# Kernel tuning notes

Hardware: AMD Instinct MI355X
Metric: run time of the kernel (lower is better)

The kernel has to match this reference:

```python
import jax, jax.numpy as jnp
import numpy as np
import math

N_NODES = 50000
N_EDGES = 500000
D = 128
H = 8
HD = D // H
N_RELS = 200


def setup_inputs() -> dict:
    key = jax.random.key(0)
    ks = jax.random.split(key, 12)
    return {
        "q": jax.random.normal(ks[0], (N_NODES, D), jnp.float32),
        "E": jax.random.normal(ks[1], (N_NODES, D), jnp.float32),
        "R_emb": jax.random.normal(ks[2], (N_RELS, D), jnp.float32),
        "Wq": jax.random.normal(ks[3], (D, D), jnp.float32) / math.sqrt(D),
        "Wk": jax.random.normal(ks[4], (D, D), jnp.float32) / math.sqrt(D),
        "Wv": jax.random.normal(ks[5], (D, D), jnp.float32) / math.sqrt(D),
        "Wo": jax.random.normal(ks[6], (4 * D, D), jnp.float32) / math.sqrt(4 * D),
        "ln_g": jnp.ones((D,), jnp.float32),
        "ln_b": jnp.zeros((D,), jnp.float32),
        "deg_scale": jax.random.uniform(ks[7], (N_EDGES,), jnp.float32) + 0.5,
        "edge_src": jax.random.randint(ks[8], (N_EDGES,), 0, N_NODES),
        "edge_rel": jax.random.randint(ks[9], (N_EDGES,), 0, N_RELS),
        "edge_dst": jax.random.randint(ks[10], (N_EDGES,), 0, N_NODES),
    }


def reference(q, E, R_emb, Wq, Wk, Wv, Wo, ln_g, ln_b, deg_scale,
              edge_src, edge_rel, edge_dst):
    n = q.shape[0]
    # DistMult message: ent * rel per edge   [E, D]
    msg = E[edge_src] * R_emb[edge_rel]
    # scatter multi-head sigmoid attention (query_expand = edge_dst)
    k = (msg @ Wk).reshape(-1, H, HD)                      # [E, H, hd]
    qe = (q @ Wq)[edge_dst].reshape(-1, H, HD)             # [E, H, hd]
    alphas = (qe * k).sum(-1) / math.sqrt(HD)              # [E, H]
    w = jax.nn.sigmoid(alphas)                             # sigmoid attention
    v = (msg @ Wv).reshape(-1, H, HD)                      # [E, H, hd]
    scaled_v = (w[..., None] * v).reshape(-1, D)           # [E, D]
    # simple_pna: scalars={'scaled'} (v * deg_scale), aggs=[mean,max,min,std]
    x = scaled_v * deg_scale[:, None]                      # [E, D]
    seg = edge_dst
    s = jax.ops.segment_sum(x, seg, num_segments=n)        # sum
    cnt = jax.ops.segment_sum(jnp.ones((x.shape[0],), x.dtype), seg, num_segments=n)
    nonempty = (cnt > 0)[:, None]
    mean = jnp.where(nonempty, s / jnp.maximum(cnt, 1.0)[:, None], 0.0)
    mx = jax.ops.segment_max(x, seg, num_segments=n)
    mx = jnp.where(nonempty, mx, 0.0)                      # empty segs -> 0 (torch zeros init)
    mn = jax.ops.segment_min(x, seg, num_segments=n)
    mn = jnp.where(nonempty, mn, 0.0)
    sq = jax.ops.segment_sum(x * x, seg, num_segments=n)
    std = jnp.sqrt(jnp.maximum(sq - s * s, 1e-8))          # matches (sq_agg - sum_agg**2).clamp_min(1e-8).sqrt()
    agg = jnp.concatenate([mean, mx, mn, std], axis=-1)    # [N, 4D]
    out = agg @ Wo                                         # [N, D]
    # GatedResidueNorm, use_gate=False: residual add + LayerNorm
    h = out + q
    mu = h.mean(-1, keepdims=True)
    var = ((h - mu) ** 2).mean(-1, keepdims=True)
    return (h - mu) * jax.lax.rsqrt(var + 1e-5) * ln_g + ln_b
```

## Files before the change

kernel.cpp:

```cpp
#include <hip/hip_runtime.h>

#define D 128

typedef __attribute__((ext_vector_type(8))) short short8;
typedef __attribute__((ext_vector_type(4))) float floatx4;

union __align__(16) U8 { unsigned short u[8]; short8 v; };

__device__ __forceinline__ unsigned enc_f(float f) {
    unsigned u = __float_as_uint(f);
    return (u & 0x80000000u) ? ~u : (u | 0x80000000u);
}
__device__ __forceinline__ float dec_f(unsigned u) {
    return (u & 0x80000000u) ? __uint_as_float(u ^ 0x80000000u) : __uint_as_float(~u);
}
__device__ __forceinline__ unsigned short f2bf(float f) {
    unsigned u = __float_as_uint(f);
    unsigned r = (u + 0x7FFFu + ((u >> 16) & 1u)) >> 16;
    return (unsigned short)r;
}
__device__ __forceinline__ float bf2f(unsigned short s) {
    return __uint_as_float(((unsigned)s) << 16);
}


__global__ void init_kernel(float* __restrict__ sum, float* __restrict__ sumsq,
                            unsigned* __restrict__ mxe, unsigned* __restrict__ mne,
                            int* __restrict__ cnt, int* __restrict__ fill, int nNodes) {
    int i = blockIdx.x * blockDim.x + threadIdx.x;
    int total = nNodes * D;
    if (i < total) {
        sum[i] = 0.f;
        sumsq[i] = 0.f;
        mxe[i] = 0u;
        mne[i] = 0xFFFFFFFFu;
    }
    if (i < nNodes) { cnt[i] = 0; fill[i] = 0; }
}


__global__ void hist_kernel(const int* __restrict__ dst, int* __restrict__ cnt, int nE) {
    int i = blockIdx.x * blockDim.x + threadIdx.x;
    if (i < nE) atomicAdd(&cnt[dst[i]], 1);
}

__global__ void scanA_kernel(const int* __restrict__ cnt, int* __restrict__ chunksum, int n) {
    __shared__ int sm[256];
    int t = threadIdx.x;
    int i = blockIdx.x * 256 + t;
    sm[t] = (i < n) ? cnt[i] : 0;
    __syncthreads();
    for (int s = 128; s > 0; s >>= 1) {
        if (t < s) sm[t] += sm[t + s];
        __syncthreads();
    }
    if (t == 0) chunksum[blockIdx.x] = sm[0];
}

__global__ void scanB_kernel(const int* __restrict__ chunksum, int* __restrict__ chunkoff, int nc) {
    __shared__ int sm[256];
    int t = threadIdx.x;
    int v = (t < nc) ? chunksum[t] : 0;
    sm[t] = v;
    __syncthreads();
    for (int s = 1; s < 256; s <<= 1) {
        int add = (t >= s) ? sm[t - s] : 0;
        __syncthreads();
        sm[t] += add;
        __syncthreads();
    }
    if (t < nc) chunkoff[t] = sm[t] - v;
}

__global__ void scanC_kernel(const int* __restrict__ cnt, const int* __restrict__ chunkoff,
                             int* __restrict__ off, int n) {
    __shared__ int sm[256];
    int t = threadIdx.x;
    int i = blockIdx.x * 256 + t;
    int v = (i < n) ? cnt[i] : 0;
    sm[t] = v;
    __syncthreads();
    for (int s = 1; s < 256; s <<= 1) {
        int add = (t >= s) ? sm[t - s] : 0;
        __syncthreads();
        sm[t] += add;
        __syncthreads();
    }
    if (i < n) off[i] = chunkoff[blockIdx.x] + sm[t] - v;
}

__global__ void scatter_kernel(const int* __restrict__ dst, const int* __restrict__ off,
                               int* __restrict__ fill, int* __restrict__ perm, int nE) {
    int i = blockIdx.x * blockDim.x + threadIdx.x;
    if (i < nE) {
        int d = dst[i];
        int p = off[d] + atomicAdd(&fill[d], 1);
        perm[p] = i;
    }
}


__global__ void pack_kernel(const float* __restrict__ W0, const float* __restrict__ W1,
                            int Kdim, unsigned short* __restrict__ hi,
                            unsigned short* __restrict__ lo) {
    int ksn = Kdim >> 5;
    int nt = blockIdx.x / ksn;
    int ks = blockIdx.x % ksn;
    int l = threadIdx.x;
    int c = nt * 16 + (l & 15);
    const float* Wsrc = (c < 128) ? W0 : W1;
    int cc = c & 127;
    int kbase = ks * 32 + (l >> 4) * 8;
    size_t o = ((size_t)blockIdx.x * 64 + l) * 8;
#pragma unroll
    for (int j = 0; j < 8; ++j) {
        float w = Wsrc[(size_t)(kbase + j) * 128 + cc];
        unsigned short h = f2bf(w);
        hi[o + j] = h;
        if (lo) lo[o + j] = f2bf(w - bf2f(h));
    }
}


__global__ __launch_bounds__(256, 2) void qproj_mfma(
        const float* __restrict__ q,
        const unsigned short* __restrict__ Bhi, const unsigned short* __restrict__ Blo,
        unsigned short* __restrict__ qp, int nNodes) {
    __shared__ __align__(16) unsigned short qhi[64][128];
    __shared__ __align__(16) unsigned short qlo[64][128];
    int t = threadIdx.x;
    int n0 = blockIdx.x * 64;
    {
        int e = t >> 2, sub = t & 3;
        int node = n0 + e;
        for (int cc = 0; cc < 4; ++cc) {
            int chunk = sub * 4 + cc;
            U8 H, L;
            if (node < nNodes) {
                const float* srcp = q + (size_t)node * 128 + chunk * 8;
                float4 v0 = *(const float4*)(srcp);
                float4 v1 = *(const float4*)(srcp + 4);
                float vv[8] = {v0.x, v0.y, v0.z, v0.w, v1.x, v1.y, v1.z, v1.w};
#pragma unroll
                for (int j = 0; j < 8; ++j) {
                    unsigned short h = f2bf(vv[j]);
                    H.u[j] = h; L.u[j] = f2bf(vv[j] - bf2f(h));
                }
            } else {
#pragma unroll
                for (int j = 0; j < 8; ++j) { H.u[j] = 0; L.u[j] = 0; }
            }
            int sc = chunk ^ (e & 7);
            *reinterpret_cast<short8*>(&qhi[e][sc * 8]) = H.v;
            *reinterpret_cast<short8*>(&qlo[e][sc * 8]) = L.v;
        }
    }
    __syncthreads();
    int w = t >> 6, l = t & 63;
    int lrow = l & 15, lk = l >> 4;
    floatx4 acc[4][2];
#pragma unroll
    for (int mt = 0; mt < 4; ++mt)
#pragma unroll
        for (int n = 0; n < 2; ++n) acc[mt][n] = (floatx4){0.f, 0.f, 0.f, 0.f};
    for (int ks = 0; ks < 4; ++ks) {
        short8 ah[4], al[4];
#pragma unroll
        for (int mt = 0; mt < 4; ++mt) {
            int row = mt * 16 + lrow;
            int sc = (ks * 4 + lk) ^ (row & 7);
            ah[mt] = *reinterpret_cast<const short8*>(&qhi[row][sc * 8]);
            al[mt] = *reinterpret_cast<const short8*>(&qlo[row][sc * 8]);
        }
#pragma unroll
        for (int ntl = 0; ntl < 2; ++ntl) {
            int ntg = w * 2 + ntl;
            size_t bo = ((size_t)(ntg * 4 + ks) * 64 + l) * 8;
            short8 bh = *reinterpret_cast<const short8*>(Bhi + bo);
            short8 bl = *reinterpret_cast<const short8*>(Blo + bo);
#pragma unroll
            for (int mt = 0; mt < 4; ++mt) {
                acc[mt][ntl] = __builtin_amdgcn_mfma_f32_16x16x32_bf16(ah[mt], bh, acc[mt][ntl], 0, 0, 0);
                acc[mt][ntl] = __builtin_amdgcn_mfma_f32_16x16x32_bf16(al[mt], bh, acc[mt][ntl], 0, 0, 0);
                acc[mt][ntl] = __builtin_amdgcn_mfma_f32_16x16x32_bf16(ah[mt], bl, acc[mt][ntl], 0, 0, 0);
            }
        }
    }
#pragma unroll
    for (int mt = 0; mt < 4; ++mt)
#pragma unroll
        for (int ntl = 0; ntl < 2; ++ntl) {
            int col = (w * 2 + ntl) * 16 + lrow;
#pragma unroll
            for (int r = 0; r < 4; ++r) {
                int row = mt * 16 + lk * 4 + r;
                int node = n0 + row;
                if (node < nNodes) qp[(size_t)node * 128 + col] = f2bf(acc[mt][ntl][r]);
            }
        }
}


__device__ __forceinline__ void flush1(float* __restrict__ sum, float* __restrict__ sumsq,
                                       unsigned* __restrict__ mxe, unsigned* __restrict__ mne,
                                       int node, int col, float s, float q2, float mx, float mn) {
    size_t b = (size_t)node * 128 + col;
    atomicAdd(&sum[b], s);
    atomicAdd(&sumsq[b], q2);
    atomicMax(&mxe[b], enc_f(mx));
    atomicMin(&mne[b], enc_f(mn));
}

__global__ __launch_bounds__(256, 2) void edge_mfma(
        const float* __restrict__ E, const float* __restrict__ R,
        const unsigned short* __restrict__ qp,
        const unsigned short* __restrict__ Bhi, const unsigned short* __restrict__ Blo,
        const float* __restrict__ deg,
        const int* __restrict__ src, const int* __restrict__ rel,
        const int* __restrict__ dst, const int* __restrict__ perm,
        float* __restrict__ sum, float* __restrict__ sumsq,
        unsigned* __restrict__ mxe, unsigned* __restrict__ mne, int nE) {

    __shared__ __align__(16) unsigned short msgb[2][64][128];
    __shared__ __align__(16) unsigned short Kb[64][128];
    __shared__ float alph[64][8];
    __shared__ int sdst[64];
    __shared__ float sdegs[64];

    int t = threadIdx.x;
    int e0 = blockIdx.x * 64;

    if (t < 64) {
        int ei = e0 + t;
        if (ei < nE) { int p = perm[ei]; sdst[t] = dst[p]; sdegs[t] = deg[p]; }
        else { sdst[t] = -1; sdegs[t] = 0.f; }
    }
    {
        int e = t >> 2, sub = t & 3;
        int ei = e0 + e;
        bool ok = ei < nE;
        int p = ok ? perm[ei] : 0;
        const float* Erow = E + (size_t)(ok ? src[p] : 0) * 128;
        const float* Rrow = R + (size_t)(ok ? rel[p] : 0) * 128;
        for (int cc = 0; cc < 4; ++cc) {
            int chunk = sub * 4 + cc;
            U8 H, L;
            if (ok) {
                float4 a0 = *(const float4*)(Erow + chunk * 8);
                float4 a1 = *(const float4*)(Erow + chunk * 8 + 4);
                float4 b0 = *(const float4*)(Rrow + chunk * 8);
                float4 b1 = *(const float4*)(Rrow + chunk * 8 + 4);
                float m[8] = {a0.x * b0.x, a0.y * b0.y, a0.z * b0.z, a0.w * b0.w,
                              a1.x * b1.x, a1.y * b1.y, a1.z * b1.z, a1.w * b1.w};
#pragma unroll
                for (int j = 0; j < 8; ++j) {
                    unsigned short h = f2bf(m[j]);
                    H.u[j] = h; L.u[j] = f2bf(m[j] - bf2f(h));
                }
            } else {
#pragma unroll
                for (int j = 0; j < 8; ++j) { H.u[j] = 0; L.u[j] = 0; }
            }
            int sc = chunk ^ (e & 7);
            *reinterpret_cast<short8*>(&msgb[0][e][sc * 8]) = H.v;
            *reinterpret_cast<short8*>(&msgb[1][e][sc * 8]) = L.v;
        }
    }
    __syncthreads();

    int w = t >> 6, l = t & 63;
    int lrow = l & 15, lk = l >> 4;
    int colbase = w * 64;
    floatx4 acc[4][4];
#pragma unroll
    for (int mt = 0; mt < 4; ++mt)
#pragma unroll
        for (int n = 0; n < 4; ++n) acc[mt][n] = (floatx4){0.f, 0.f, 0.f, 0.f};

    for (int ks = 0; ks < 4; ++ks) {
        short8 ah[4], al[4];
#pragma unroll
        for (int mt = 0; mt < 4; ++mt) {
            int row = mt * 16 + lrow;
            int sc = (ks * 4 + lk) ^ (row & 7);
            ah[mt] = *reinterpret_cast<const short8*>(&msgb[0][row][sc * 8]);
            al[mt] = *reinterpret_cast<const short8*>(&msgb[1][row][sc * 8]);
        }
#pragma unroll
        for (int ntl = 0; ntl < 4; ++ntl) {
            int ntg = w * 4 + ntl;
            size_t bo = ((size_t)(ntg * 4 + ks) * 64 + l) * 8;
            short8 bh = *reinterpret_cast<const short8*>(Bhi + bo);
            short8 bl = *reinterpret_cast<const short8*>(Blo + bo);
#pragma unroll
            for (int mt = 0; mt < 4; ++mt) {
                acc[mt][ntl] = __builtin_amdgcn_mfma_f32_16x16x32_bf16(ah[mt], bh, acc[mt][ntl], 0, 0, 0);
                acc[mt][ntl] = __builtin_amdgcn_mfma_f32_16x16x32_bf16(al[mt], bh, acc[mt][ntl], 0, 0, 0);
                acc[mt][ntl] = __builtin_amdgcn_mfma_f32_16x16x32_bf16(ah[mt], bl, acc[mt][ntl], 0, 0, 0);
            }
        }
    }
    __syncthreads();

    float* Vlds = (float*)msgb;
#pragma unroll
    for (int mt = 0; mt < 4; ++mt)
#pragma unroll
        for (int ntl = 0; ntl < 4; ++ntl) {
            int col = colbase + ntl * 16 + lrow;
#pragma unroll
            for (int r = 0; r < 4; ++r) {
                int row = mt * 16 + lk * 4 + r;
                int key = ((row >> 2) & 3) << 4;
                float vvv = acc[mt][ntl][r];
                if (col < 128) Kb[row][col ^ key] = f2bf(vvv);
                else Vlds[row * 128 + ((col - 128) ^ key)] = vvv;
            }
        }
    __syncthreads();

    {
        int e = t >> 2, h2 = (t & 3) * 2;
        int dn = sdst[e];
        int key = ((e >> 2) & 3) << 4;
#pragma unroll
        for (int hh = 0; hh < 2; ++hh) {
            int h = h2 + hh;
            float wgt = 0.f;
            if (dn >= 0) {
                int cb = (h * 16) ^ key;
                U8 k0, k1, q0, q1;
                k0.v = *reinterpret_cast<const short8*>(&Kb[e][cb]);
                k1.v = *reinterpret_cast<const short8*>(&Kb[e][cb + 8]);
                const unsigned short* qrow = qp + (size_t)dn * 128 + h * 16;
                q0.v = *reinterpret_cast<const short8*>(qrow);
                q1.v = *reinterpret_cast<const short8*>(qrow + 8);
                float a = 0.f;
#pragma unroll
                for (int j = 0; j < 8; ++j) {
                    a = fmaf(bf2f(k0.u[j]), bf2f(q0.u[j]), a);
                    a = fmaf(bf2f(k1.u[j]), bf2f(q1.u[j]), a);
                }
                float alpha = a * 0.25f;
                wgt = 1.f / (1.f + __expf(-alpha));
            }
            alph[e][h] = wgt;
        }
    }
    __syncthreads();

    {
        int col = t & 127, seg = t >> 7;
        int eb = seg * 32, ee = eb + 32;
        float s = 0.f, q2 = 0.f, mx = 0.f, mn = 0.f;
        int run = -1;
        for (int e = eb; e < ee; ++e) {
            int dnv = sdst[e];
            if (dnv < 0) {
                if (run >= 0) { flush1(sum, sumsq, mxe, mne, run, col, s, q2, mx, mn); run = -1; }
                continue;
            }
            int key = ((e >> 2) & 3) << 4;
            float x = Vlds[e * 128 + (col ^ key)] * alph[e][col >> 4] * sdegs[e];
            if (dnv != run) {
                if (run >= 0) flush1(sum, sumsq, mxe, mne, run, col, s, q2, mx, mn);
                run = dnv;
                s = x; q2 = x * x; mx = x; mn = x;
            } else {
                s += x; q2 = fmaf(x, x, q2);
                mx = fmaxf(mx, x); mn = fminf(mn, x);
            }
        }
        if (run >= 0) flush1(sum, sumsq, mxe, mne, run, col, s, q2, mx, mn);
    }
}


__global__ __launch_bounds__(256, 2) void finalize_mfma(
        const float* __restrict__ sum, const float* __restrict__ sumsq,
        const unsigned* __restrict__ mxe, const unsigned* __restrict__ mne,
        const int* __restrict__ cnt, const unsigned short* __restrict__ Wop,
        const float* __restrict__ q, const float* __restrict__ ln_g,
        const float* __restrict__ ln_b, float* __restrict__ out, int nNodes) {
    __shared__ __align__(16) unsigned short aggb[32][512];
    int t = threadIdx.x;
    int n0 = blockIdx.x * 32;
    {
        int nl = t >> 3, part = t & 7;
        int node = n0 + nl;
        int c0 = part * 16;
        U8 Mh[2], Xh[2], Nh[2], Sh[2];
        if (node < nNodes) {
            int c = cnt[node];
            float invc = (c > 0) ? 1.f / (float)c : 0.f;
            size_t b0 = (size_t)node * 128 + c0;
#pragma unroll
            for (int g = 0; g < 2; ++g) {
                float4 s0 = *(const float4*)(sum + b0 + g * 8);
                float4 s1 = *(const float4*)(sum + b0 + g * 8 + 4);
                float4 t0 = *(const float4*)(sumsq + b0 + g * 8);
                float4 t1 = *(const float4*)(sumsq + b0 + g * 8 + 4);
                uint4 x0 = *(const uint4*)(mxe + b0 + g * 8);
                uint4 x1 = *(const uint4*)(mxe + b0 + g * 8 + 4);
                uint4 m0 = *(const uint4*)(mne + b0 + g * 8);
                uint4 m1 = *(const uint4*)(mne + b0 + g * 8 + 4);
                float ss[8] = {s0.x, s0.y, s0.z, s0.w, s1.x, s1.y, s1.z, s1.w};
                float qq[8] = {t0.x, t0.y, t0.z, t0.w, t1.x, t1.y, t1.z, t1.w};
                unsigned xx[8] = {x0.x, x0.y, x0.z, x0.w, x1.x, x1.y, x1.z, x1.w};
                unsigned nn[8] = {m0.x, m0.y, m0.z, m0.w, m1.x, m1.y, m1.z, m1.w};
#pragma unroll
                for (int j = 0; j < 8; ++j) {
                    float s = ss[j];
                    float mean = s * invc;
                    float mxv = (c > 0) ? dec_f(xx[j]) : 0.f;
                    float mnv = (c > 0) ? dec_f(nn[j]) : 0.f;
                    float sd = sqrtf(fmaxf(qq[j] - s * s, 1e-8f));
                    Mh[g].u[j] = f2bf(mean);
                    Xh[g].u[j] = f2bf(mxv);
                    Nh[g].u[j] = f2bf(mnv);
                    Sh[g].u[j] = f2bf(sd);
                }
            }
        } else {
#pragma unroll
            for (int g = 0; g < 2; ++g)
#pragma unroll
                for (int j = 0; j < 8; ++j) { Mh[g].u[j] = 0; Xh[g].u[j] = 0; Nh[g].u[j] = 0; Sh[g].u[j] = 0; }
        }
#pragma unroll
        for (int g = 0; g < 2; ++g) {
            int base = part * 2 + g, k = nl & 7, ch;
            ch = (0 * 16 + base) ^ k; *reinterpret_cast<short8*>(&aggb[nl][ch * 8]) = Mh[g].v;
            ch = (1 * 16 + base) ^ k; *reinterpret_cast<short8*>(&aggb[nl][ch * 8]) = Xh[g].v;
            ch = (2 * 16 + base) ^ k; *reinterpret_cast<short8*>(&aggb[nl][ch * 8]) = Nh[g].v;
            ch = (3 * 16 + base) ^ k; *reinterpret_cast<short8*>(&aggb[nl][ch * 8]) = Sh[g].v;
        }
    }
    __syncthreads();

    int w = t >> 6, l = t & 63;
    int lrow = l & 15, lk = l >> 4;
    floatx4 acc[2][2];
#pragma unroll
    for (int mt = 0; mt < 2; ++mt)
#pragma unroll
        for (int n = 0; n < 2; ++n) acc[mt][n] = (floatx4){0.f, 0.f, 0.f, 0.f};
    for (int ks = 0; ks < 16; ++ks) {
        short8 a[2];
#pragma unroll
        for (int mt = 0; mt < 2; ++mt) {
            int row = mt * 16 + lrow;
            int ch = (ks * 4 + lk) ^ (row & 7);
            a[mt] = *reinterpret_cast<const short8*>(&aggb[row][ch * 8]);
        }
#pragma unroll
        for (int ntl = 0; ntl < 2; ++ntl) {
            int ntg = w * 2 + ntl;
            short8 b = *reinterpret_cast<const short8*>(Wop + ((size_t)(ntg * 16 + ks) * 64 + l) * 8);
#pragma unroll
            for (int mt = 0; mt < 2; ++mt)
                acc[mt][ntl] = __builtin_amdgcn_mfma_f32_16x16x32_bf16(a[mt], b, acc[mt][ntl], 0, 0, 0);
        }
    }
    __syncthreads();

    float* hb = (float*)aggb;
#pragma unroll
    for (int mt = 0; mt < 2; ++mt)
#pragma unroll
        for (int ntl = 0; ntl < 2; ++ntl) {
            int col = (w * 2 + ntl) * 16 + lrow;
#pragma unroll
            for (int r = 0; r < 4; ++r) {
                int row = mt * 16 + lk * 4 + r;
                int node = n0 + row;
                float h = acc[mt][ntl][r] + ((node < nNodes) ? q[(size_t)node * 128 + col] : 0.f);
                int key = ((row >> 2) & 3) << 4;
                hb[row * 128 + (col ^ key)] = h;
            }
        }
    __syncthreads();

    {
        int nl = t >> 3, part = t & 7;
        int node = n0 + nl;
        int key = ((nl >> 2) & 3) << 4;
        int c0 = part * 16;
        int cb = c0 ^ key;
        const float* hrow = hb + nl * 128;
        float4 h0 = *(const float4*)(hrow + cb);
        float4 h1 = *(const float4*)(hrow + cb + 4);
        float4 h2 = *(const float4*)(hrow + cb + 8);
        float4 h3 = *(const float4*)(hrow + cb + 12);
        float ps = h0.x + h0.y + h0.z + h0.w + h1.x + h1.y + h1.z + h1.w
                 + h2.x + h2.y + h2.z + h2.w + h3.x + h3.y + h3.z + h3.w;
        ps += __shfl_xor(ps, 1);
        ps += __shfl_xor(ps, 2);
        ps += __shfl_xor(ps, 4);
        float mu = ps * (1.f / 128.f);
        float d0x = h0.x - mu, d0y = h0.y - mu, d0z = h0.z - mu, d0w = h0.w - mu;
        float d1x = h1.x - mu, d1y = h1.y - mu, d1z = h1.z - mu, d1w = h1.w - mu;
        float d2x = h2.x - mu, d2y = h2.y - mu, d2z = h2.z - mu, d2w = h2.w - mu;
        float d3x = h3.x - mu, d3y = h3.y - mu, d3z = h3.z - mu, d3w = h3.w - mu;
        float pv = d0x*d0x + d0y*d0y + d0z*d0z + d0w*d0w
                 + d1x*d1x + d1y*d1y + d1z*d1z + d1w*d1w
                 + d2x*d2x + d2y*d2y + d2z*d2z + d2w*d2w
                 + d3x*d3x + d3y*d3y + d3z*d3z + d3w*d3w;
        pv += __shfl_xor(pv, 1);
        pv += __shfl_xor(pv, 2);
        pv += __shfl_xor(pv, 4);
        float rr = rsqrtf(pv * (1.f / 128.f) + 1e-5f);
        if (node < nNodes) {
            float4 g0 = *(const float4*)(ln_g + c0);
            float4 g1 = *(const float4*)(ln_g + c0 + 4);
            float4 g2 = *(const float4*)(ln_g + c0 + 8);
            float4 g3 = *(const float4*)(ln_g + c0 + 12);
            float4 b0 = *(const float4*)(ln_b + c0);
            float4 b1 = *(const float4*)(ln_b + c0 + 4);
            float4 b2 = *(const float4*)(ln_b + c0 + 8);
            float4 b3 = *(const float4*)(ln_b + c0 + 12);
            float* orow = out + (size_t)node * 128 + c0;
            float4 o;
            o.x = d0x * rr * g0.x + b0.x; o.y = d0y * rr * g0.y + b0.y;
            o.z = d0z * rr * g0.z + b0.z; o.w = d0w * rr * g0.w + b0.w;
            *(float4*)(orow) = o;
            o.x = d1x * rr * g1.x + b1.x; o.y = d1y * rr * g1.y + b1.y;
            o.z = d1z * rr * g1.z + b1.z; o.w = d1w * rr * g1.w + b1.w;
            *(float4*)(orow + 4) = o;
            o.x = d2x * rr * g2.x + b2.x; o.y = d2y * rr * g2.y + b2.y;
            o.z = d2z * rr * g2.z + b2.z; o.w = d2w * rr * g2.w + b2.w;
            *(float4*)(orow + 8) = o;
            o.x = d3x * rr * g3.x + b3.x; o.y = d3y * rr * g3.y + b3.y;
            o.z = d3z * rr * g3.z + b3.z; o.w = d3w * rr * g3.w + b3.w;
            *(float4*)(orow + 12) = o;
        }
    }
}


extern "C" void kernel_launch(void* const* d_in, const int* in_sizes, int n_in,
                              void* d_out, int out_size, void* d_ws, size_t ws_size,
                              hipStream_t stream) {
    const float* q    = (const float*)d_in[0];
    const float* E    = (const float*)d_in[1];
    const float* R    = (const float*)d_in[2];
    const float* Wq   = (const float*)d_in[3];
    const float* Wk   = (const float*)d_in[4];
    const float* Wv   = (const float*)d_in[5];
    const float* Wo   = (const float*)d_in[6];
    const float* ln_g = (const float*)d_in[7];
    const float* ln_b = (const float*)d_in[8];
    const float* deg  = (const float*)d_in[9];
    const int* src    = (const int*)d_in[10];
    const int* rel    = (const int*)d_in[11];
    const int* dst    = (const int*)d_in[12];
    int nNodes = in_sizes[0] / D;
    int nEdges = in_sizes[10];
    float* out = (float*)d_out;

    char* w = (char*)d_ws;
    size_t nd = (size_t)nNodes * D;
    float* sum    = (float*)w;               w += nd * 4;
    float* sumsq  = (float*)w;               w += nd * 4;
    unsigned* mxe = (unsigned*)w;            w += nd * 4;
    unsigned* mne = (unsigned*)w;            w += nd * 4;
    unsigned short* qp = (unsigned short*)w; w += nd * 2;
    int* cnt      = (int*)w;                 w += (size_t)nNodes * 4;
    int* off      = (int*)w;                 w += (size_t)nNodes * 4;
    int* fill     = (int*)w;                 w += (size_t)nNodes * 4;
    int* perm     = (int*)w;                 w += (size_t)nEdges * 4;
    int* chunksum = (int*)w;                 w += 256 * 4;
    int* chunkoff = (int*)w;                 w += 256 * 4;
    unsigned short* Wp_hi  = (unsigned short*)w; w += 16 * 4 * 64 * 8 * 2;
    unsigned short* Wp_lo  = (unsigned short*)w; w += 16 * 4 * 64 * 8 * 2;
    unsigned short* Wqp_hi = (unsigned short*)w; w += 8 * 4 * 64 * 8 * 2;
    unsigned short* Wqp_lo = (unsigned short*)w; w += 8 * 4 * 64 * 8 * 2;
    unsigned short* Wop    = (unsigned short*)w; w += 8 * 16 * 64 * 8 * 2;

    int nChunks = (nNodes + 255) / 256;

    init_kernel<<<(int)((nd + 255) / 256), 256, 0, stream>>>(sum, sumsq, mxe, mne, cnt, fill, nNodes);
    hist_kernel<<<(nEdges + 255) / 256, 256, 0, stream>>>(dst, cnt, nEdges);
    scanA_kernel<<<nChunks, 256, 0, stream>>>(cnt, chunksum, nNodes);
    scanB_kernel<<<1, 256, 0, stream>>>(chunksum, chunkoff, nChunks);
    scanC_kernel<<<nChunks, 256, 0, stream>>>(cnt, chunkoff, off, nNodes);
    scatter_kernel<<<(nEdges + 255) / 256, 256, 0, stream>>>(dst, off, fill, perm, nEdges);

    pack_kernel<<<16 * 4, 64, 0, stream>>>(Wk, Wv, 128, Wp_hi, Wp_lo);
    pack_kernel<<<8 * 4, 64, 0, stream>>>(Wq, Wq, 128, Wqp_hi, Wqp_lo);
    pack_kernel<<<8 * 16, 64, 0, stream>>>(Wo, Wo, 512, Wop, (unsigned short*)nullptr);

    qproj_mfma<<<(nNodes + 63) / 64, 256, 0, stream>>>(q, Wqp_hi, Wqp_lo, qp, nNodes);
    edge_mfma<<<(nEdges + 63) / 64, 256, 0, stream>>>(E, R, qp, Wp_hi, Wp_lo, deg,
                                                      src, rel, dst, perm,
                                                      sum, sumsq, mxe, mne, nEdges);
    finalize_mfma<<<(nNodes + 31) / 32, 256, 0, stream>>>(sum, sumsq, mxe, mne, cnt, Wop,
                                                          q, ln_g, ln_b, out, nNodes);
}
```

Baseline: 546.1 us.

## Fuse edge processing, aggregation and output projection into a per-node-block kernel

Replaces the edge-parallel kernel, which scattered partial aggregates into global buffers with atomics, and the separate finalize kernel with one kernel that owns 8 destination nodes per block. Each block walks its sorted edge range in chunks of 32, does the K/V MFMA and the sigmoid attention, and reduces sum, sumsq, max and min in registers. It then applies the Wo projection and LayerNorm directly. This removes the big init pass, the global atomics and the round trip of the intermediate aggregates, at the cost of uneven per-block work, small partly padded MFMA tiles, and an MFMA M-tile of 16 when only 8 rows are valid.

```diff
diff --git a/kernel.cpp b/kernel.cpp
--- a/kernel.cpp
+++ b/kernel.cpp
@@ -1,19 +1,13 @@
 #include <hip/hip_runtime.h>
 
 #define D 128
+#define FLT_BIG 3.402823466e+38f
 
 typedef __attribute__((ext_vector_type(8))) short short8;
 typedef __attribute__((ext_vector_type(4))) float floatx4;
 
 union __align__(16) U8 { unsigned short u[8]; short8 v; };
 
-__device__ __forceinline__ unsigned enc_f(float f) {
-    unsigned u = __float_as_uint(f);
-    return (u & 0x80000000u) ? ~u : (u | 0x80000000u);
-}
-__device__ __forceinline__ float dec_f(unsigned u) {
-    return (u & 0x80000000u) ? __uint_as_float(u ^ 0x80000000u) : __uint_as_float(~u);
-}
 __device__ __forceinline__ unsigned short f2bf(float f) {
     unsigned u = __float_as_uint(f);
     unsigned r = (u + 0x7FFFu + ((u >> 16) & 1u)) >> 16;
@@ -24,20 +18,10 @@
 }
 
 
-__global__ void init_kernel(float* __restrict__ sum, float* __restrict__ sumsq,
-                            unsigned* __restrict__ mxe, unsigned* __restrict__ mne,
-                            int* __restrict__ cnt, int* __restrict__ fill, int nNodes) {
+__global__ void zero2_kernel(int* __restrict__ cnt, int* __restrict__ fill, int n) {
     int i = blockIdx.x * blockDim.x + threadIdx.x;
-    int total = nNodes * D;
-    if (i < total) {
-        sum[i] = 0.f;
-        sumsq[i] = 0.f;
-        mxe[i] = 0u;
-        mne[i] = 0xFFFFFFFFu;
-    }
-    if (i < nNodes) { cnt[i] = 0; fill[i] = 0; }
-}
-
+    if (i < n) { cnt[i] = 0; fill[i] = 0; }
+}
 
 __global__ void hist_kernel(const int* __restrict__ dst, int* __restrict__ cnt, int nE) {
     int i = blockIdx.x * blockDim.x + threadIdx.x;
@@ -201,338 +185,271 @@
 }
 
 
-__device__ __forceinline__ void flush1(float* __restrict__ sum, float* __restrict__ sumsq,
-                                       unsigned* __restrict__ mxe, unsigned* __restrict__ mne,
-                                       int node, int col, float s, float q2, float mx, float mn) {
-    size_t b = (size_t)node * 128 + col;
-    atomicAdd(&sum[b], s);
-    atomicAdd(&sumsq[b], q2);
-    atomicMax(&mxe[b], enc_f(mx));
-    atomicMin(&mne[b], enc_f(mn));
-}
-
-__global__ __launch_bounds__(256, 2) void edge_mfma(
+__global__ __launch_bounds__(256, 4) void edge_fused(
         const float* __restrict__ E, const float* __restrict__ R,
         const unsigned short* __restrict__ qp,
         const unsigned short* __restrict__ Bhi, const unsigned short* __restrict__ Blo,
+        const unsigned short* __restrict__ Wop,
         const float* __restrict__ deg,
         const int* __restrict__ src, const int* __restrict__ rel,
         const int* __restrict__ dst, const int* __restrict__ perm,
-        float* __restrict__ sum, float* __restrict__ sumsq,
-        unsigned* __restrict__ mxe, unsigned* __restrict__ mne, int nE) {
-
-    __shared__ __align__(16) unsigned short msgb[2][64][128];
-    __shared__ __align__(16) unsigned short Kb[64][128];
-    __shared__ float alph[64][8];
-    __shared__ int sdst[64];
-    __shared__ float sdegs[64];
+        const int* __restrict__ off,
+        const float* __restrict__ q, const float* __restrict__ ln_g,
+        const float* __restrict__ ln_b, float* __restrict__ out,
+        int nNodes, int nE) {
+
+    __shared__ __align__(16) unsigned short msgb[2][32][128];
+    __shared__ __align__(16) unsigned short Kb[32][128];
+    __shared__ float alph[32][8];
+    __shared__ __align__(16) unsigned short qpl[8][128];
+    __shared__ float sdeg[32];
+    __shared__ int sdst[32];
+    __shared__ int noff[9];
 
     int t = threadIdx.x;
-    int e0 = blockIdx.x * 64;
-
-    if (t < 64) {
-        int ei = e0 + t;
-        if (ei < nE) { int p = perm[ei]; sdst[t] = dst[p]; sdegs[t] = deg[p]; }
-        else { sdst[t] = -1; sdegs[t] = 0.f; }
+    int n0 = blockIdx.x * 8;
+
+    if (t < 9) {
+        int idx = n0 + t;
+        noff[t] = (idx < nNodes) ? off[idx] : nE;
     }
     {
-        int e = t >> 2, sub = t & 3;
-        int ei = e0 + e;
-        bool ok = ei < nE;
-        int p = ok ? perm[ei] : 0;
-        const float* Erow = E + (size_t)(ok ? src[p] : 0) * 128;
-        const float* Rrow = R + (size_t)(ok ? rel[p] : 0) * 128;
-        for (int cc = 0; cc < 4; ++cc) {
-            int chunk = sub * 4 + cc;
-            U8 H, L;
-            if (ok) {
-                float4 a0 = *(const float4*)(Erow + chunk * 8);
-                float4 a1 = *(const float4*)(Erow + chunk * 8 + 4);
-                float4 b0 = *(const float4*)(Rrow + chunk * 8);
-                float4 b1 = *(const float4*)(Rrow + chunk * 8 + 4);
-                float m[8] = {a0.x * b0.x, a0.y * b0.y, a0.z * b0.z, a0.w * b0.w,
-                              a1.x * b1.x, a1.y * b1.y, a1.z * b1.z, a1.w * b1.w};
-#pragma unroll
-                for (int j = 0; j < 8; ++j) {
-                    unsigned short h = f2bf(m[j]);
-                    H.u[j] = h; L.u[j] = f2bf(m[j] - bf2f(h));
-                }
-            } else {
-#pragma unroll
-                for (int j = 0; j < 8; ++j) { H.u[j] = 0; L.u[j] = 0; }
-            }
-            int sc = chunk ^ (e & 7);
-            *reinterpret_cast<short8*>(&msgb[0][e][sc * 8]) = H.v;
-            *reinterpret_cast<short8*>(&msgb[1][e][sc * 8]) = L.v;
-        }
-    }
-    __syncthreads();
+        int ln = t >> 5, g = t & 31;
+        int node = n0 + ln;
+        ushort4 v;
+        if (node < nNodes) v = *(const ushort4*)(qp + (size_t)node * 128 + g * 4);
+        else { v.x = 0; v.y = 0; v.z = 0; v.w = 0; }
+        *(ushort4*)(&qpl[ln][g * 4]) = v;
+    }
+    __syncthreads();
+
+    int eb = noff[0], ee = noff[8];
+
+    int lnS = t >> 5, gS = t & 31;
+    float sSx = 0.f, sSy = 0.f, sSz = 0.f, sSw = 0.f;
+    float sQx = 0.f, sQy = 0.f, sQz = 0.f, sQw = 0.f;
+    float sXx = -FLT_BIG, sXy = -FLT_BIG, sXz = -FLT_BIG, sXw = -FLT_BIG;
+    float sNx = FLT_BIG, sNy = FLT_BIG, sNz = FLT_BIG, sNw = FLT_BIG;
 
     int w = t >> 6, l = t & 63;
     int lrow = l & 15, lk = l >> 4;
-    int colbase = w * 64;
-    floatx4 acc[4][4];
-#pragma unroll
-    for (int mt = 0; mt < 4; ++mt)
-#pragma unroll
-        for (int n = 0; n < 4; ++n) acc[mt][n] = (floatx4){0.f, 0.f, 0.f, 0.f};
-
-    for (int ks = 0; ks < 4; ++ks) {
-        short8 ah[4], al[4];
-#pragma unroll
-        for (int mt = 0; mt < 4; ++mt) {
-            int row = mt * 16 + lrow;
-            int sc = (ks * 4 + lk) ^ (row & 7);
-            ah[mt] = *reinterpret_cast<const short8*>(&msgb[0][row][sc * 8]);
-            al[mt] = *reinterpret_cast<const short8*>(&msgb[1][row][sc * 8]);
-        }
-#pragma unroll
-        for (int ntl = 0; ntl < 4; ++ntl) {
-            int ntg = w * 4 + ntl;
-            size_t bo = ((size_t)(ntg * 4 + ks) * 64 + l) * 8;
-            short8 bh = *reinterpret_cast<const short8*>(Bhi + bo);
-            short8 bl = *reinterpret_cast<const short8*>(Blo + bo);
-#pragma unroll
-            for (int mt = 0; mt < 4; ++mt) {
-                acc[mt][ntl] = __builtin_amdgcn_mfma_f32_16x16x32_bf16(ah[mt], bh, acc[mt][ntl], 0, 0, 0);
-                acc[mt][ntl] = __builtin_amdgcn_mfma_f32_16x16x32_bf16(al[mt], bh, acc[mt][ntl], 0, 0, 0);
-                acc[mt][ntl] = __builtin_amdgcn_mfma_f32_16x16x32_bf16(ah[mt], bl, acc[mt][ntl], 0, 0, 0);
-            }
-        }
-    }
-    __syncthreads();
-
     float* Vlds = (float*)msgb;
-#pragma unroll
-    for (int mt = 0; mt < 4; ++mt)
-#pragma unroll
-        for (int ntl = 0; ntl < 4; ++ntl) {
-            int col = colbase + ntl * 16 + lrow;
-#pragma unroll
-            for (int r = 0; r < 4; ++r) {
-                int row = mt * 16 + lk * 4 + r;
-                int key = ((row >> 2) & 3) << 4;
-                float vvv = acc[mt][ntl][r];
-                if (col < 128) Kb[row][col ^ key] = f2bf(vvv);
-                else Vlds[row * 128 + ((col - 128) ^ key)] = vvv;
-            }
-        }
-    __syncthreads();
-
-    {
-        int e = t >> 2, h2 = (t & 3) * 2;
-        int dn = sdst[e];
-        int key = ((e >> 2) & 3) << 4;
-#pragma unroll
-        for (int hh = 0; hh < 2; ++hh) {
-            int h = h2 + hh;
-            float wgt = 0.f;
-            if (dn >= 0) {
+
+    for (int c0 = eb; c0 < ee; c0 += 32) {
+        {
+            int e = t >> 3, sub = t & 7;
+            int ei = c0 + e;
+            bool ok = (ei < ee);
+            int p = ok ? perm[ei] : 0;
+            if (sub == 0) sdst[e] = ok ? (dst[p] - n0) : -1;
+            if (sub == 1) sdeg[e] = ok ? deg[p] : 0.f;
+            const float* Erow = E + (size_t)(ok ? src[p] : 0) * 128;
+            const float* Rrow = R + (size_t)(ok ? rel[p] : 0) * 128;
+#pragma unroll
+            for (int cc = 0; cc < 2; ++cc) {
+                int chunk = sub * 2 + cc;
+                U8 H, L;
+                if (ok) {
+                    float4 a0 = *(const float4*)(Erow + chunk * 8);
+                    float4 a1 = *(const float4*)(Erow + chunk * 8 + 4);
+                    float4 b0 = *(const float4*)(Rrow + chunk * 8);
+                    float4 b1 = *(const float4*)(Rrow + chunk * 8 + 4);
+                    float m[8] = {a0.x * b0.x, a0.y * b0.y, a0.z * b0.z, a0.w * b0.w,
+                                  a1.x * b1.x, a1.y * b1.y, a1.z * b1.z, a1.w * b1.w};
+#pragma unroll
+                    for (int j = 0; j < 8; ++j) {
+                        unsigned short h = f2bf(m[j]);
+                        H.u[j] = h; L.u[j] = f2bf(m[j] - bf2f(h));
+                    }
+                } else {
+#pragma unroll
+                    for (int j = 0; j < 8; ++j) { H.u[j] = 0; L.u[j] = 0; }
+                }
+                int sc = chunk ^ (e & 7);
+                *reinterpret_cast<short8*>(&msgb[0][e][sc * 8]) = H.v;
+                *reinterpret_cast<short8*>(&msgb[1][e][sc * 8]) = L.v;
+            }
+        }
+        __syncthreads();
+
+        floatx4 acc[2][4];
+#pragma unroll
+        for (int mt = 0; mt < 2; ++mt)
+#pragma unroll
+            for (int n = 0; n < 4; ++n) acc[mt][n] = (floatx4){0.f, 0.f, 0.f, 0.f};
+        for (int ks = 0; ks < 4; ++ks) {
+            short8 ah[2], al[2];
+#pragma unroll
+            for (int mt = 0; mt < 2; ++mt) {
+                int row = mt * 16 + lrow;
+                int sc = (ks * 4 + lk) ^ (row & 7);
+                ah[mt] = *reinterpret_cast<const short8*>(&msgb[0][row][sc * 8]);
+                al[mt] = *reinterpret_cast<const short8*>(&msgb[1][row][sc * 8]);
+            }
+#pragma unroll
+            for (int ntl = 0; ntl < 4; ++ntl) {
+                int ntg = (ntl < 2) ? (w * 2 + ntl) : (8 + w * 2 + (ntl - 2));
+                size_t bo = ((size_t)(ntg * 4 + ks) * 64 + l) * 8;
+                short8 bh = *reinterpret_cast<const short8*>(Bhi + bo);
+                short8 bl = *reinterpret_cast<const short8*>(Blo + bo);
+#pragma unroll
+                for (int mt = 0; mt < 2; ++mt) {
+                    acc[mt][ntl] = __builtin_amdgcn_mfma_f32_16x16x32_bf16(ah[mt], bh, acc[mt][ntl], 0, 0, 0);
+                    acc[mt][ntl] = __builtin_amdgcn_mfma_f32_16x16x32_bf16(al[mt], bh, acc[mt][ntl], 0, 0, 0);
+                    acc[mt][ntl] = __builtin_amdgcn_mfma_f32_16x16x32_bf16(ah[mt], bl, acc[mt][ntl], 0, 0, 0);
+                }
+            }
+        }
+        __syncthreads();
+
+#pragma unroll
+        for (int mt = 0; mt < 2; ++mt)
+#pragma unroll
+            for (int ntl = 0; ntl < 4; ++ntl) {
+                int ntg = (ntl < 2) ? (w * 2 + ntl) : (8 + w * 2 + (ntl - 2));
+                int col = ntg * 16 + lrow;
+#pragma unroll
+                for (int r = 0; r < 4; ++r) {
+                    int row = mt * 16 + lk * 4 + r;
+                    int key = ((row >> 2) & 3) << 4;
+                    float v = acc[mt][ntl][r];
+                    if (col < 128) Kb[row][col ^ key] = f2bf(v);
+                    else Vlds[row * 128 + ((col - 128) ^ key)] = v;
+                }
+            }
+        __syncthreads();
+
+        {
+            int e = t >> 3, h = t & 7;
+            int ln = sdst[e];
+            float wv = 0.f;
+            if (ln >= 0) {
+                int key = ((e >> 2) & 3) << 4;
                 int cb = (h * 16) ^ key;
                 U8 k0, k1, q0, q1;
                 k0.v = *reinterpret_cast<const short8*>(&Kb[e][cb]);
                 k1.v = *reinterpret_cast<const short8*>(&Kb[e][cb + 8]);
-                const unsigned short* qrow = qp + (size_t)dn * 128 + h * 16;
-                q0.v = *reinterpret_cast<const short8*>(qrow);
-                q1.v = *reinterpret_cast<const short8*>(qrow + 8);
+                q0.v = *reinterpret_cast<const short8*>(&qpl[ln][h * 16]);
+                q1.v = *reinterpret_cast<const short8*>(&qpl[ln][h * 16 + 8]);
                 float a = 0.f;
 #pragma unroll
                 for (int j = 0; j < 8; ++j) {
                     a = fmaf(bf2f(k0.u[j]), bf2f(q0.u[j]), a);
                     a = fmaf(bf2f(k1.u[j]), bf2f(q1.u[j]), a);
                 }
-                float alpha = a * 0.25f;
-                wgt = 1.f / (1.f + __expf(-alpha));
-            }
-            alph[e][h] = wgt;
-        }
-    }
-    __syncthreads();
-
+                float alphav = a * 0.25f;
+                wv = sdeg[e] / (1.f + __expf(-alphav));
+            }
+            alph[e][h] = wv;
+        }
+        __syncthreads();
+
+        {
+            int lo = max(noff[lnS], c0);
+            int hi = min(noff[lnS + 1], c0 + 32);
+            for (int ei2 = lo; ei2 < hi; ++ei2) {
+                int el = ei2 - c0;
+                int key = ((el >> 2) & 3) << 4;
+                float4 v4 = *(const float4*)(Vlds + el * 128 + ((gS * 4) ^ key));
+                float aa = alph[el][gS >> 2];
+                float xx = v4.x * aa, xy = v4.y * aa, xz = v4.z * aa, xw = v4.w * aa;
+                sSx += xx; sSy += xy; sSz += xz; sSw += xw;
+                sQx = fmaf(xx, xx, sQx); sQy = fmaf(xy, xy, sQy);
+                sQz = fmaf(xz, xz, sQz); sQw = fmaf(xw, xw, sQw);
+                sXx = fmaxf(sXx, xx); sXy = fmaxf(sXy, xy);
+                sXz = fmaxf(sXz, xz); sXw = fmaxf(sXw, xw);
+                sNx = fminf(sNx, xx); sNy = fminf(sNy, xy);
+                sNz = fminf(sNz, xz); sNw = fminf(sNw, xw);
+            }
+        }
+        __syncthreads();
+    }
+
+    unsigned short* aggb = (unsigned short*)msgb;
+    *reinterpret_cast<short8*>(aggb + 8 * 512 + t * 16) = (short8){0,0,0,0,0,0,0,0};
+    *reinterpret_cast<short8*>(aggb + 8 * 512 + t * 16 + 8) = (short8){0,0,0,0,0,0,0,0};
     {
-        int col = t & 127, seg = t >> 7;
-        int eb = seg * 32, ee = eb + 32;
-        float s = 0.f, q2 = 0.f, mx = 0.f, mn = 0.f;
-        int run = -1;
-        for (int e = eb; e < ee; ++e) {
-            int dnv = sdst[e];
-            if (dnv < 0) {
-                if (run >= 0) { flush1(sum, sumsq, mxe, mne, run, col, s, q2, mx, mn); run = -1; }
-                continue;
-            }
-            int key = ((e >> 2) & 3) << 4;
-            float x = Vlds[e * 128 + (col ^ key)] * alph[e][col >> 4] * sdegs[e];
-            if (dnv != run) {
-                if (run >= 0) flush1(sum, sumsq, mxe, mne, run, col, s, q2, mx, mn);
-                run = dnv;
-                s = x; q2 = x * x; mx = x; mn = x;
-            } else {
-                s += x; q2 = fmaf(x, x, q2);
-                mx = fmaxf(mx, x); mn = fminf(mn, x);
-            }
-        }
-        if (run >= 0) flush1(sum, sumsq, mxe, mne, run, col, s, q2, mx, mn);
-    }
-}
-
-
-__global__ __launch_bounds__(256, 2) void finalize_mfma(
-        const float* __restrict__ sum, const float* __restrict__ sumsq,
-        const unsigned* __restrict__ mxe, const unsigned* __restrict__ mne,
-        const int* __restrict__ cnt, const unsigned short* __restrict__ Wop,
-        const float* __restrict__ q, const float* __restrict__ ln_g,
-        const float* __restrict__ ln_b, float* __restrict__ out, int nNodes) {
-    __shared__ __align__(16) unsigned short aggb[32][512];
-    int t = threadIdx.x;
-    int n0 = blockIdx.x * 32;
-    {
-        int nl = t >> 3, part = t & 7;
-        int node = n0 + nl;
-        int c0 = part * 16;
-        U8 Mh[2], Xh[2], Nh[2], Sh[2];
-        if (node < nNodes) {
-            int c = cnt[node];
-            float invc = (c > 0) ? 1.f / (float)c : 0.f;
-            size_t b0 = (size_t)node * 128 + c0;
-#pragma unroll
-            for (int g = 0; g < 2; ++g) {
-                float4 s0 = *(const float4*)(sum + b0 + g * 8);
-                float4 s1 = *(const float4*)(sum + b0 + g * 8 + 4);
-                float4 t0 = *(const float4*)(sumsq + b0 + g * 8);
-                float4 t1 = *(const float4*)(sumsq + b0 + g * 8 + 4);
-                uint4 x0 = *(const uint4*)(mxe + b0 + g * 8);
-                uint4 x1 = *(const uint4*)(mxe + b0 + g * 8 + 4);
-                uint4 m0 = *(const uint4*)(mne + b0 + g * 8);
-                uint4 m1 = *(const uint4*)(mne + b0 + g * 8 + 4);
-                float ss[8] = {s0.x, s0.y, s0.z, s0.w, s1.x, s1.y, s1.z, s1.w};
-                float qq[8] = {t0.x, t0.y, t0.z, t0.w, t1.x, t1.y, t1.z, t1.w};
-                unsigned xx[8] = {x0.x, x0.y, x0.z, x0.w, x1.x, x1.y, x1.z, x1.w};
-                unsigned nn[8] = {m0.x, m0.y, m0.z, m0.w, m1.x, m1.y, m1.z, m1.w};
-#pragma unroll
-                for (int j = 0; j < 8; ++j) {
-                    float s = ss[j];
-                    float mean = s * invc;
-                    float mxv = (c > 0) ? dec_f(xx[j]) : 0.f;
-                    float mnv = (c > 0) ? dec_f(nn[j]) : 0.f;
-                    float sd = sqrtf(fmaxf(qq[j] - s * s, 1e-8f));
-                    Mh[g].u[j] = f2bf(mean);
-                    Xh[g].u[j] = f2bf(mxv);
-                    Nh[g].u[j] = f2bf(mnv);
-                    Sh[g].u[j] = f2bf(sd);
-                }
-            }
-        } else {
-#pragma unroll
-            for (int g = 0; g < 2; ++g)
-#pragma unroll
-                for (int j = 0; j < 8; ++j) { Mh[g].u[j] = 0; Xh[g].u[j] = 0; Nh[g].u[j] = 0; Sh[g].u[j] = 0; }
-        }
-#pragma unroll
-        for (int g = 0; g < 2; ++g) {
-            int base = part * 2 + g, k = nl & 7, ch;
-            ch = (0 * 16 + base) ^ k; *reinterpret_cast<short8*>(&aggb[nl][ch * 8]) = Mh[g].v;
-            ch = (1 * 16 + base) ^ k; *reinterpret_cast<short8*>(&aggb[nl][ch * 8]) = Xh[g].v;
-            ch = (2 * 16 + base) ^ k; *reinterpret_cast<short8*>(&aggb[nl][ch * 8]) = Nh[g].v;
-            ch = (3 * 16 + base) ^ k; *reinterpret_cast<short8*>(&aggb[nl][ch * 8]) = Sh[g].v;
-        }
-    }
-    __syncthreads();
-
-    int w = t >> 6, l = t & 63;
-    int lrow = l & 15, lk = l >> 4;
-    floatx4 acc[2][2];
-#pragma unroll
-    for (int mt = 0; mt < 2; ++mt)
-#pragma unroll
-        for (int n = 0; n < 2; ++n) acc[mt][n] = (floatx4){0.f, 0.f, 0.f, 0.f};
+        int c = noff[lnS + 1] - noff[lnS];
+        float invc = (c > 0) ? 1.f / (float)c : 0.f;
+        float vals[4][4];
+        vals[0][0] = sSx * invc; vals[0][1] = sSy * invc; vals[0][2] = sSz * invc; vals[0][3] = sSw * invc;
+        vals[1][0] = (c > 0) ? sXx : 0.f; vals[1][1] = (c > 0) ? sXy : 0.f;
+        vals[1][2] = (c > 0) ? sXz : 0.f; vals[1][3] = (c > 0) ? sXw : 0.f;
+        vals[2][0] = (c > 0) ? sNx : 0.f; vals[2][1] = (c > 0) ? sNy : 0.f;
+        vals[2][2] = (c > 0) ? sNz : 0.f; vals[2][3] = (c > 0) ? sNw : 0.f;
+        vals[3][0] = sqrtf(fmaxf(sQx - sSx * sSx, 1e-8f));
+        vals[3][1] = sqrtf(fmaxf(sQy - sSy * sSy, 1e-8f));
+        vals[3][2] = sqrtf(fmaxf(sQz - sSz * sSz, 1e-8f));
+        vals[3][3] = sqrtf(fmaxf(sQw - sSw * sSw, 1e-8f));
+#pragma unroll
+        for (int s = 0; s < 4; ++s) {
+            int chunk = s * 16 + (gS >> 1);
+            int pos = ((chunk ^ (lnS & 7)) << 3) + ((gS & 1) * 4);
+            ushort4 o;
+            o.x = f2bf(vals[s][0]); o.y = f2bf(vals[s][1]);
+            o.z = f2bf(vals[s][2]); o.w = f2bf(vals[s][3]);
+            *(ushort4*)(aggb + lnS * 512 + pos) = o;
+        }
+    }
+    __syncthreads();
+
+    floatx4 acc2[2];
+    acc2[0] = (floatx4){0.f, 0.f, 0.f, 0.f};
+    acc2[1] = (floatx4){0.f, 0.f, 0.f, 0.f};
     for (int ks = 0; ks < 16; ++ks) {
-        short8 a[2];
-#pragma unroll
-        for (int mt = 0; mt < 2; ++mt) {
-            int row = mt * 16 + lrow;
-            int ch = (ks * 4 + lk) ^ (row & 7);
-            a[mt] = *reinterpret_cast<const short8*>(&aggb[row][ch * 8]);
-        }
+        int sc = (ks * 4 + lk) ^ (lrow & 7);
+        short8 a = *reinterpret_cast<const short8*>(aggb + lrow * 512 + sc * 8);
 #pragma unroll
         for (int ntl = 0; ntl < 2; ++ntl) {
             int ntg = w * 2 + ntl;
             short8 b = *reinterpret_cast<const short8*>(Wop + ((size_t)(ntg * 16 + ks) * 64 + l) * 8);
-#pragma unroll
-            for (int mt = 0; mt < 2; ++mt)
-                acc[mt][ntl] = __builtin_amdgcn_mfma_f32_16x16x32_bf16(a[mt], b, acc[mt][ntl], 0, 0, 0);
-        }
-    }
-    __syncthreads();
-
-    float* hb = (float*)aggb;
-#pragma unroll
-    for (int mt = 0; mt < 2; ++mt)
-#pragma unroll
-        for (int ntl = 0; ntl < 2; ++ntl) {
-            int col = (w * 2 + ntl) * 16 + lrow;
-#pragma unroll
-            for (int r = 0; r < 4; ++r) {
-                int row = mt * 16 + lk * 4 + r;
+            acc2[ntl] = __builtin_amdgcn_mfma_f32_16x16x32_bf16(a, b, acc2[ntl], 0, 0, 0);
+        }
+    }
+
+    float* hb = (float*)Kb;
+#pragma unroll
+    for (int ntl = 0; ntl < 2; ++ntl) {
+        int col = (w * 2 + ntl) * 16 + lrow;
+#pragma unroll
+        for (int r = 0; r < 4; ++r) {
+            int row = lk * 4 + r;
+            if (row < 8) {
                 int node = n0 + row;
-                float h = acc[mt][ntl][r] + ((node < nNodes) ? q[(size_t)node * 128 + col] : 0.f);
-                int key = ((row >> 2) & 3) << 4;
-                hb[row * 128 + (col ^ key)] = h;
-            }
-        }
+                float h = acc2[ntl][r] + ((node < nNodes) ? q[(size_t)node * 128 + col] : 0.f);
+                hb[row * 128 + col] = h;
+            }
+        }
+    }
     __syncthreads();
 
     {
-        int nl = t >> 3, part = t & 7;
-        int node = n0 + nl;
-        int key = ((nl >> 2) & 3) << 4;
-        int c0 = part * 16;
-        int cb = c0 ^ key;
-        const float* hrow = hb + nl * 128;
-        float4 h0 = *(const float4*)(hrow + cb);
-        float4 h1 = *(const float4*)(hrow + cb + 4);
-        float4 h2 = *(const float4*)(hrow + cb + 8);
-        float4 h3 = *(const float4*)(hrow + cb + 12);
-        float ps = h0.x + h0.y + h0.z + h0.w + h1.x + h1.y + h1.z + h1.w
-                 + h2.x + h2.y + h2.z + h2.w + h3.x + h3.y + h3.z + h3.w;
+        int node = n0 + lnS;
+        float4 h4 = *(const float4*)(hb + lnS * 128 + gS * 4);
+        float ps = h4.x + h4.y + h4.z + h4.w;
         ps += __shfl_xor(ps, 1);
         ps += __shfl_xor(ps, 2);
         ps += __shfl_xor(ps, 4);
+        ps += __shfl_xor(ps, 8);
+        ps += __shfl_xor(ps, 16);
         float mu = ps * (1.f / 128.f);
-        float d0x = h0.x - mu, d0y = h0.y - mu, d0z = h0.z - mu, d0w = h0.w - mu;
-        float d1x = h1.x - mu, d1y = h1.y - mu, d1z = h1.z - mu, d1w = h1.w - mu;
-        float d2x = h2.x - mu, d2y = h2.y - mu, d2z = h2.z - mu, d2w = h2.w - mu;
-        float d3x = h3.x - mu, d3y = h3.y - mu, d3z = h3.z - mu, d3w = h3.w - mu;
-        float pv = d0x*d0x + d0y*d0y + d0z*d0z + d0w*d0w
-                 + d1x*d1x + d1y*d1y + d1z*d1z + d1w*d1w
-                 + d2x*d2x + d2y*d2y + d2z*d2z + d2w*d2w
-                 + d3x*d3x + d3y*d3y + d3z*d3z + d3w*d3w;
+        float dx = h4.x - mu, dy = h4.y - mu, dz = h4.z - mu, dw = h4.w - mu;
+        float pv = dx * dx + dy * dy + dz * dz + dw * dw;
         pv += __shfl_xor(pv, 1);
         pv += __shfl_xor(pv, 2);
         pv += __shfl_xor(pv, 4);
+        pv += __shfl_xor(pv, 8);
+        pv += __shfl_xor(pv, 16);
         float rr = rsqrtf(pv * (1.f / 128.f) + 1e-5f);
         if (node < nNodes) {
-            float4 g0 = *(const float4*)(ln_g + c0);
-            float4 g1 = *(const float4*)(ln_g + c0 + 4);
-            float4 g2 = *(const float4*)(ln_g + c0 + 8);
-            float4 g3 = *(const float4*)(ln_g + c0 + 12);
-            float4 b0 = *(const float4*)(ln_b + c0);
-            float4 b1 = *(const float4*)(ln_b + c0 + 4);
-            float4 b2 = *(const float4*)(ln_b + c0 + 8);
-            float4 b3 = *(const float4*)(ln_b + c0 + 12);
-            float* orow = out + (size_t)node * 128 + c0;
+            float4 gv = *(const float4*)(ln_g + gS * 4);
+            float4 bv = *(const float4*)(ln_b + gS * 4);
             float4 o;
-            o.x = d0x * rr * g0.x + b0.x; o.y = d0y * rr * g0.y + b0.y;
-            o.z = d0z * rr * g0.z + b0.z; o.w = d0w * rr * g0.w + b0.w;
-            *(float4*)(orow) = o;
-            o.x = d1x * rr * g1.x + b1.x; o.y = d1y * rr * g1.y + b1.y;
-            o.z = d1z * rr * g1.z + b1.z; o.w = d1w * rr * g1.w + b1.w;
-            *(float4*)(orow + 4) = o;
-            o.x = d2x * rr * g2.x + b2.x; o.y = d2y * rr * g2.y + b2.y;
-            o.z = d2z * rr * g2.z + b2.z; o.w = d2w * rr * g2.w + b2.w;
-            *(float4*)(orow + 8) = o;
-            o.x = d3x * rr * g3.x + b3.x; o.y = d3y * rr * g3.y + b3.y;
-            o.z = d3z * rr * g3.z + b3.z; o.w = d3w * rr * g3.w + b3.w;
-            *(float4*)(orow + 12) = o;
+            o.x = dx * rr * gv.x + bv.x;
+            o.y = dy * rr * gv.y + bv.y;
+            o.z = dz * rr * gv.z + bv.z;
+            o.w = dw * rr * gv.w + bv.w;
+            *(float4*)(out + (size_t)node * 128 + gS * 4) = o;
         }
     }
 }
@@ -560,10 +477,6 @@
 
     char* w = (char*)d_ws;
     size_t nd = (size_t)nNodes * D;
-    float* sum    = (float*)w;               w += nd * 4;
-    float* sumsq  = (float*)w;               w += nd * 4;
-    unsigned* mxe = (unsigned*)w;            w += nd * 4;
-    unsigned* mne = (unsigned*)w;            w += nd * 4;
     unsigned short* qp = (unsigned short*)w; w += nd * 2;
     int* cnt      = (int*)w;                 w += (size_t)nNodes * 4;
     int* off      = (int*)w;                 w += (size_t)nNodes * 4;
@@ -579,7 +492,7 @@
 
     int nChunks = (nNodes + 255) / 256;
 
-    init_kernel<<<(int)((nd + 255) / 256), 256, 0, stream>>>(sum, sumsq, mxe, mne, cnt, fill, nNodes);
+    zero2_kernel<<<(nNodes + 255) / 256, 256, 0, stream>>>(cnt, fill, nNodes);
     hist_kernel<<<(nEdges + 255) / 256, 256, 0, stream>>>(dst, cnt, nEdges);
     scanA_kernel<<<nChunks, 256, 0, stream>>>(cnt, chunksum, nNodes);
     scanB_kernel<<<1, 256, 0, stream>>>(chunksum, chunkoff, nChunks);
@@ -591,9 +504,7 @@
     pack_kernel<<<8 * 16, 64, 0, stream>>>(Wo, Wo, 512, Wop, (unsigned short*)nullptr);
 
     qproj_mfma<<<(nNodes + 63) / 64, 256, 0, stream>>>(q, Wqp_hi, Wqp_lo, qp, nNodes);
-    edge_mfma<<<(nEdges + 63) / 64, 256, 0, stream>>>(E, R, qp, Wp_hi, Wp_lo, deg,
-                                                      src, rel, dst, perm,
-                                                      sum, sumsq, mxe, mne, nEdges);
-    finalize_mfma<<<(nNodes + 31) / 32, 256, 0, stream>>>(sum, sumsq, mxe, mne, cnt, Wop,
-                                                          q, ln_g, ln_b, out, nNodes);
-}
+    edge_fused<<<(nNodes + 7) / 8, 256, 0, stream>>>(E, R, qp, Wp_hi, Wp_lo, Wop, deg,
+                                                     src, rel, dst, perm, off,
+                                                     q, ln_g, ln_b, out, nNodes, nEdges);
+}
```

New measurement: 784.3 us. +43.6%, slower.
